# Performance work log

Measured on AMD Instinct MI355X. Metric: run time of the kernel, lower is better.

## Reference

```python
import jax, jax.numpy as jnp
import numpy as np

N_NODES = 50000
N_EDGES = 800000
N_HIDDEN = 64
N_LAYER = 3
IN_DIM = 4


def setup_inputs() -> dict:
    key = jax.random.key(0)
    ks = jax.random.split(key, 10)
    x = jax.random.normal(ks[0], (N_NODES, IN_DIM), dtype=jnp.float32)
    edge_index = jax.random.randint(ks[1], (2, N_EDGES), 0, N_NODES, dtype=jnp.int64)
    # Glorot-style params matching pyg GCNConv (lin has no bias; conv adds bias after aggregation)
    def glorot(k, fan_in, fan_out):
        s = jnp.sqrt(6.0 / (fan_in + fan_out))
        return jax.random.uniform(k, (fan_in, fan_out), jnp.float32, -s, s)
    W_in = glorot(ks[2], IN_DIM, N_HIDDEN)
    b_in = jnp.zeros((N_HIDDEN,), jnp.float32)
    W_h = jnp.stack([glorot(jax.random.fold_in(ks[3], i), N_HIDDEN, N_HIDDEN) for i in range(N_LAYER)])
    b_h = jnp.zeros((N_LAYER, N_HIDDEN), jnp.float32)
    W_out = glorot(ks[4], N_HIDDEN, 1)
    b_out = jnp.zeros((1,), jnp.float32)
    return {"x": x, "edge_index": edge_index, "W_in": W_in, "b_in": b_in,
            "W_h": W_h, "b_h": b_h, "W_out": W_out, "b_out": b_out}


def _gcn_norm(edge_index, n_nodes):
    # add self-loops, compute symmetric norm D^{-1/2} (A+I) D^{-1/2}
    loop = jnp.arange(n_nodes, dtype=edge_index.dtype)
    src = jnp.concatenate([edge_index[0], loop])
    dst = jnp.concatenate([edge_index[1], loop])
    deg = jax.ops.segment_sum(jnp.ones_like(dst, dtype=jnp.float32), dst, num_segments=n_nodes)
    dinv = jax.lax.rsqrt(deg)  # deg >= 1 due to self-loops
    norm = dinv[src] * dinv[dst]
    return src, dst, norm


def _gcn_conv(x, W, b, src, dst, norm, n_nodes):
    h = x @ W                                   # [N, out]
    msg = h[src] * norm[:, None]                # gather + scale, [E+N, out]
    out = jax.ops.segment_sum(msg, dst, num_segments=n_nodes)  # scatter-add
    return out + b


def reference(x, edge_index, W_in, b_in, W_h, b_h, W_out, b_out):
    n = x.shape[0]
    src, dst, norm = _gcn_norm(edge_index, n)
    h = jax.nn.relu(_gcn_conv(x, W_in, b_in, src, dst, norm, n))
    for i in range(W_h.shape[0]):
        h = jax.nn.relu(_gcn_conv(h, W_h[i], b_h[i], src, dst, norm, n))
    return _gcn_conv(h, W_out, b_out, src, dst, norm, n)
```

## Files before the change

kernel.cpp:

```cpp
#include <hip/hip_runtime.h>
#include <hip/hip_bf16.h>


#define TPB 256
#define EPT 8
#define CHUNK (TPB * EPT)
typedef __hip_bfloat16 bf16;
#define B2F __bfloat162float

__global__ void k_zero_b(int* __restrict__ bktcnt, int* __restrict__ ticket) {
    bktcnt[threadIdx.x] = 0;
    if (threadIdx.x == 0) *ticket = 0;
}

__global__ __launch_bounds__(TPB) void k_bktcnt(
    const int* __restrict__ dst, int* __restrict__ bktcnt, int* __restrict__ ticket,
    int* __restrict__ bktbase, int* __restrict__ bcur, int E, int n) {
    __shared__ int h[256];
    __shared__ int lastFlag;
    int tid = threadIdx.x;
    h[tid] = 0;
    __syncthreads();
    int e0 = blockIdx.x * CHUNK;
#pragma unroll
    for (int u = 0; u < EPT; ++u) {
        int e = e0 + u * TPB + tid;
        if (e < E) {
            int d = dst[e];
            if ((unsigned)d < (unsigned)n) atomicAdd(&h[d >> 8], 1);
        }
    }
    __syncthreads();
    if (h[tid]) atomicAdd(&bktcnt[tid], h[tid]);
    __threadfence();
    __syncthreads();
    if (tid == 0) lastFlag = (atomicAdd(ticket, 1) == (int)gridDim.x - 1);
    __syncthreads();
    if (!lastFlag) return;
    int v = atomicAdd(&bktcnt[tid], 0);
    h[tid] = v;
    __syncthreads();
    for (int off = 1; off < 256; off <<= 1) {
        int u2 = (tid >= off) ? h[tid - off] : 0;
        __syncthreads();
        h[tid] += u2;
        __syncthreads();
    }
    int excl = h[tid] - v;
    bktbase[tid] = excl;
    bcur[tid] = excl;
    if (tid == 255) bktbase[256] = h[tid];
}

__global__ __launch_bounds__(TPB) void k_bin(
    const int* __restrict__ src, const int* __restrict__ dst,
    int* __restrict__ bcur, unsigned* __restrict__ staging, int E, int n) {
    __shared__ int hcnt[256];
    __shared__ int hbase[256];
    int tid = threadIdx.x;
    int e0 = blockIdx.x * CHUNK;
    hcnt[tid] = 0;
    __syncthreads();

    int eb[EPT];
    unsigned rec[EPT];
#pragma unroll
    for (int u = 0; u < EPT; ++u) {
        int e = e0 + u * TPB + tid;
        eb[u] = -1;
        if (e < E) {
            int d = dst[e], s = src[e];
            if ((unsigned)d < (unsigned)n && (unsigned)s < (unsigned)n) {
                eb[u] = d >> 8;
                rec[u] = (unsigned)s | ((unsigned)(d & 255) << 16);
                atomicAdd(&hcnt[eb[u]], 1);
            }
        }
    }
    __syncthreads();
    int c = hcnt[tid];
    hbase[tid] = (c > 0) ? atomicAdd(&bcur[tid], c) : 0;
    hcnt[tid] = 0;
    __syncthreads();
#pragma unroll
    for (int u = 0; u < EPT; ++u) {
        if (eb[u] >= 0) {
            int r = atomicAdd(&hcnt[eb[u]], 1);
            int pos = hbase[eb[u]] + r;
            if ((unsigned)pos < (unsigned)E) staging[pos] = rec[u];
        }
    }
}

__global__ __launch_bounds__(TPB) void k_unbin2(
    const unsigned* __restrict__ staging, const int* __restrict__ bktbase,
    const float* __restrict__ x, float4* __restrict__ xt,
    int* __restrict__ row_start, float* __restrict__ dinv,
    unsigned short* __restrict__ bucket, int E, int n) {
    __shared__ int cnt[256];
    __shared__ int scn[256];
    __shared__ int cur[256];
    int b = blockIdx.x, tid = threadIdx.x;
    int lo = bktbase[b], hi = bktbase[b + 1];
    lo = max(0, min(lo, E)); hi = max(lo, min(hi, E));

    cnt[tid] = 0;
    __syncthreads();
    for (int i = lo + tid; i < hi; i += TPB)
        atomicAdd(&cnt[(staging[i] >> 16) & 255], 1);
    __syncthreads();

    int v = cnt[tid];
    scn[tid] = v;
    __syncthreads();
    for (int off = 1; off < 256; off <<= 1) {
        int u = (tid >= off) ? scn[tid - off] : 0;
        __syncthreads();
        scn[tid] += u;
        __syncthreads();
    }
    int excl = scn[tid] - v;
    int base = min(lo + excl, E);
    cur[tid] = base;
    int d = (b << 8) + tid;
    if (d < n) {
        row_start[d] = base;
        float di = rsqrtf((float)v + 1.0f);
        dinv[d] = di;
        float4 xv = ((const float4*)x)[d];
        xv.x *= di; xv.y *= di; xv.z *= di; xv.w *= di;
        xt[d] = xv;
        if (d == n - 1) row_start[n] = min(base + v, E);
    }
    __syncthreads();

    for (int i = lo + tid; i < hi; i += TPB) {
        unsigned r = staging[i];
        int t = (r >> 16) & 255;
        int pos = atomicAdd(&cur[t], 1);
        if ((unsigned)pos < (unsigned)E) bucket[pos] = (unsigned short)(r & 0xffffu);
    }
}

__device__ __forceinline__ void acc_oct(float* a, uint4 w) {
    a[0] += __uint_as_float(w.x << 16);
    a[1] += __uint_as_float(w.x & 0xffff0000u);
    a[2] += __uint_as_float(w.y << 16);
    a[3] += __uint_as_float(w.y & 0xffff0000u);
    a[4] += __uint_as_float(w.z << 16);
    a[5] += __uint_as_float(w.z & 0xffff0000u);
    a[6] += __uint_as_float(w.w << 16);
    a[7] += __uint_as_float(w.w & 0xffff0000u);
}

__device__ __forceinline__ void agg_oct(const bf16* __restrict__ g,
                                        const unsigned short* __restrict__ bucket,
                                        int k0, int k1, int d, float* __restrict__ a,
                                        int lane, unsigned nm1, unsigned Em1) {
    int grp = lane >> 3, i = lane & 7;
#pragma unroll
    for (int m = 0; m < 8; ++m) a[m] = 0.f;
    if (grp == 0) {
        uint4 w = *(const uint4*)(g + (size_t)d * 64 + 8 * i);
        acc_oct(a, w);
    }
    for (int base = k0; base < k1; base += 64) {
        int cnt = min(64, k1 - base);
        int rec = bucket[min((unsigned)(base + lane), Em1)];
        int k = 0;
        for (; k + 16 <= cnt; k += 16) {
            unsigned s0 = min((unsigned)__shfl(rec, k + grp), nm1);
            unsigned s1 = min((unsigned)__shfl(rec, k + 8 + grp), nm1);
            uint4 w0 = *(const uint4*)(g + (size_t)s0 * 64 + 8 * i);
            uint4 w1 = *(const uint4*)(g + (size_t)s1 * 64 + 8 * i);
            acc_oct(a, w0);
            acc_oct(a, w1);
        }
        for (; k < cnt; k += 8) {
            int e = k + grp;
            unsigned s = min((unsigned)__shfl(rec, min(e, 63)), nm1);
            uint4 w = *(const uint4*)(g + (size_t)s * 64 + 8 * i);
            if (e < cnt) acc_oct(a, w);
        }
    }
}

__global__ __launch_bounds__(TPB, 4) void k_gconv1(
    const float4* __restrict__ xt, const float* __restrict__ dinv,
    const int* __restrict__ row_start, const unsigned short* __restrict__ bucket,
    const float* __restrict__ W_in, const float* __restrict__ b_in,
    const float* __restrict__ Wh0, bf16* __restrict__ gOut, int n, int E) {
    __shared__ float sAct[4][64];
    int tid = threadIdx.x;
    int r = tid >> 6, j = tid & 63;
    unsigned nm1 = (unsigned)(n - 1);

    float wreg[64];
#pragma unroll
    for (int k = 0; k < 64; ++k) wreg[k] = Wh0[k * 64 + j];
    float win0 = W_in[0 * 64 + j], win1 = W_in[1 * 64 + j];
    float win2 = W_in[2 * 64 + j], win3 = W_in[3 * 64 + j];
    float bj = b_in[j];

    int nw = gridDim.x * 4;
    for (int d = blockIdx.x * 4 + r; d < n; d += nw) {
        float dd = dinv[d];
        int k0 = row_start[d], k1 = row_start[d + 1];
        k1 = min(k1, E); k0 = max(min(k0, k1), 0);

        float4 v = make_float4(0.f, 0.f, 0.f, 0.f);
        if (j == 0) v = xt[d];
        for (int k = k0 + j; k < k1; k += 64) {
            unsigned s = min((unsigned)bucket[k], nm1);
            float4 t = xt[s];
            v.x += t.x; v.y += t.y; v.z += t.z; v.w += t.w;
        }
#pragma unroll
        for (int off = 1; off < 64; off <<= 1) {
            v.x += __shfl_xor(v.x, off);
            v.y += __shfl_xor(v.y, off);
            v.z += __shfl_xor(v.z, off);
            v.w += __shfl_xor(v.w, off);
        }
        float dot = fmaf(v.x, win0, fmaf(v.y, win1, fmaf(v.z, win2, v.w * win3)));
        float act = fmaxf(fmaf(dd, dot, bj), 0.f);
        sAct[r][j] = act;

        float acc0 = 0.f, acc1 = 0.f, acc2 = 0.f, acc3 = 0.f;
        const float4* ap = (const float4*)&sAct[r][0];
#pragma unroll
        for (int k4 = 0; k4 < 16; ++k4) {
            float4 av = ap[k4];
            acc0 = fmaf(av.x, wreg[4 * k4 + 0], acc0);
            acc1 = fmaf(av.y, wreg[4 * k4 + 1], acc1);
            acc2 = fmaf(av.z, wreg[4 * k4 + 2], acc2);
            acc3 = fmaf(av.w, wreg[4 * k4 + 3], acc3);
        }
        float acc = (acc0 + acc1) + (acc2 + acc3);
        gOut[(size_t)d * 64 + j] = __float2bfloat16(acc * dd);
    }
}

__global__ __launch_bounds__(TPB, 4) void k_gconv(
    const bf16* __restrict__ gIn, const float* __restrict__ dinv,
    const int* __restrict__ row_start, const unsigned short* __restrict__ bucket,
    const float* __restrict__ bias, const float* __restrict__ W,
    bf16* __restrict__ gOut, int n, int E) {
    __shared__ float sVp[4][8][68];
    int tid = threadIdx.x;
    int r = tid >> 6, j = tid & 63;
    int grp = j >> 3, i = j & 7;
    unsigned nm1 = (unsigned)(n - 1), Em1 = (unsigned)(E - 1);

    float wreg[64];
#pragma unroll
    for (int k = 0; k < 64; ++k) wreg[k] = W[k * 64 + j];
    float bj = bias[j];

    int nw = gridDim.x * 4;
    for (int d = blockIdx.x * 4 + r; d < n; d += nw) {
        float dd = dinv[d];
        int k0 = row_start[d], k1 = row_start[d + 1];
        k1 = min(k1, E); k0 = max(min(k0, k1), 0);

        float a[8];
        agg_oct(gIn, bucket, k0, k1, d, a, j, nm1, Em1);

        float4* prow = (float4*)&sVp[r][grp][8 * i];
        prow[0] = make_float4(a[0], a[1], a[2], a[3]);
        prow[1] = make_float4(a[4], a[5], a[6], a[7]);
        float full = 0.f;
#pragma unroll
        for (int g = 0; g < 8; ++g) full += sVp[r][g][j];

        float act = fmaxf(fmaf(dd, full, bj), 0.f);
        sVp[r][0][j] = act;

        float acc0 = 0.f, acc1 = 0.f, acc2 = 0.f, acc3 = 0.f;
#pragma unroll
        for (int k4 = 0; k4 < 16; ++k4) {
            float4 av = *(const float4*)&sVp[r][0][4 * k4];
            acc0 = fmaf(av.x, wreg[4 * k4 + 0], acc0);
            acc1 = fmaf(av.y, wreg[4 * k4 + 1], acc1);
            acc2 = fmaf(av.z, wreg[4 * k4 + 2], acc2);
            acc3 = fmaf(av.w, wreg[4 * k4 + 3], acc3);
        }
        float acc = (acc0 + acc1) + (acc2 + acc3);
        gOut[(size_t)d * 64 + j] = __float2bfloat16(acc * dd);
    }
}

__global__ __launch_bounds__(TPB) void k_gconv_z(
    const bf16* __restrict__ gIn, const float* __restrict__ dinv,
    const int* __restrict__ row_start, const unsigned short* __restrict__ bucket,
    const float* __restrict__ bias, const float* __restrict__ Wout,
    float* __restrict__ zg, int n, int E) {
    __shared__ float sVp[4][8][68];
    int tid = threadIdx.x;
    int r = tid >> 6, j = tid & 63;
    int grp = j >> 3, i = j & 7;
    int d = blockIdx.x * 4 + r;
    if (d >= n) return;
    float dd = dinv[d];
    int k0 = row_start[d], k1 = row_start[d + 1];
    k1 = min(k1, E); k0 = max(min(k0, k1), 0);

    float a[8];
    agg_oct(gIn, bucket, k0, k1, d, a, j, (unsigned)(n - 1), (unsigned)(E - 1));

    float4* prow = (float4*)&sVp[r][grp][8 * i];
    prow[0] = make_float4(a[0], a[1], a[2], a[3]);
    prow[1] = make_float4(a[4], a[5], a[6], a[7]);
    float full = 0.f;
#pragma unroll
    for (int g = 0; g < 8; ++g) full += sVp[r][g][j];

    float p = fmaxf(fmaf(dd, full, bias[j]), 0.f) * Wout[j];
#pragma unroll
    for (int off = 32; off > 0; off >>= 1) p += __shfl_down(p, off);
    if (j == 0) zg[d] = p * dd;
}

__global__ __launch_bounds__(TPB) void k_out(
    const float* __restrict__ zg, const float* __restrict__ dinv,
    const int* __restrict__ row_start, const unsigned short* __restrict__ bucket,
    const float* __restrict__ b_out, float* __restrict__ out, int n, int E) {
    int t = blockIdx.x * blockDim.x + threadIdx.x;
    int d = t >> 6, lane = t & 63;
    if (d >= n) return;
    int k0 = row_start[d], k1 = row_start[d + 1];
    k1 = min(k1, E); k0 = max(min(k0, k1), 0);
    unsigned nm1 = (unsigned)(n - 1);
    float v = 0.f;
    for (int k = k0 + lane; k < k1; k += 64) {
        unsigned s = min((unsigned)bucket[k], nm1);
        v += zg[s];
    }
#pragma unroll
    for (int off = 32; off > 0; off >>= 1) v += __shfl_down(v, off);
    if (lane == 0) out[d] = fmaf(zg[d] + v, dinv[d], b_out[0]);
}

extern "C" void kernel_launch(void* const* d_in, const int* in_sizes, int n_in,
                              void* d_out, int out_size, void* d_ws, size_t ws_size,
                              hipStream_t stream) {
    const float* x     = (const float*)d_in[0];
    const int*   ei    = (const int*)d_in[1];
    const float* W_in  = (const float*)d_in[2];
    const float* b_in  = (const float*)d_in[3];
    const float* W_h   = (const float*)d_in[4];
    const float* b_h   = (const float*)d_in[5];
    const float* W_out = (const float*)d_in[6];
    const float* b_out = (const float*)d_in[7];
    float* out = (float*)d_out;

    int N = in_sizes[0] / 4;
    int E = in_sizes[1] / 2;
    const int* src = ei;
    const int* dst = ei + E;

    char* ws = (char*)d_ws;
    bf16* gA               = (bf16*)ws;           ws += (size_t)N * 64 * 2;
    bf16* gB               = (bf16*)ws;           ws += (size_t)N * 64 * 2;
    float4* xt             = (float4*)ws;         ws += (size_t)N * 16;
    unsigned short* bucket = (unsigned short*)ws; ws += (size_t)E * 2;
    unsigned* staging      = (unsigned*)ws;       ws += (size_t)E * 4;
    int*  row_start        = (int*)ws;            ws += (size_t)(N + 1) * 4;
    float* dinv            = (float*)ws;          ws += (size_t)N * 4;
    float* zg              = (float*)ws;          ws += (size_t)N * 4;
    int*  bktcnt           = (int*)ws;            ws += 256 * 4;
    int*  ticket           = (int*)ws;            ws += 4;
    int*  bktbase          = (int*)ws;            ws += 257 * 4;
    int*  bcur             = (int*)ws;

    int B     = (N + 255) >> 8;
    int gN4   = (N + 3) / 4;
    int gPers = 1024;
    int gBin  = (E + CHUNK - 1) / CHUNK;

    k_zero_b<<<1, 256, 0, stream>>>(bktcnt, ticket);
    k_bktcnt<<<gBin, TPB, 0, stream>>>(dst, bktcnt, ticket, bktbase, bcur, E, N);
    k_bin<<<gBin, TPB, 0, stream>>>(src, dst, bcur, staging, E, N);
    k_unbin2<<<B, TPB, 0, stream>>>(staging, bktbase, x, xt, row_start, dinv, bucket, E, N);

    k_gconv1<<<gPers, TPB, 0, stream>>>(xt, dinv, row_start, bucket, W_in, b_in, W_h, gB, N, E);
    k_gconv<<<gPers, TPB, 0, stream>>>(gB, dinv, row_start, bucket, b_h, W_h + 4096, gA, N, E);
    k_gconv<<<gPers, TPB, 0, stream>>>(gA, dinv, row_start, bucket, b_h + 64, W_h + 8192, gB, N, E);
    k_gconv_z<<<gN4, TPB, 0, stream>>>(gB, dinv, row_start, bucket, b_h + 128, W_out, zg, N, E);
    k_out<<<gN4, TPB, 0, stream>>>(zg, dinv, row_start, bucket, b_out, out, N, E);
}
```

Measured before the change: 260.0 us.

## Process two destination nodes per wavefront to overlap gather latency

Each wavefront in the hidden-layer and final aggregation kernels now handles a pair of destination nodes, interleaving their neighbor gathers so that four independent row loads are in flight per iteration instead of two. The aim is more memory-level parallelism on the latency-bound sparse gather. k_gconv_z also becomes a persistent grid-stride kernel with a fixed grid of 1024 blocks. The cost is higher register pressure from two accumulator sets, plus extra tail loops when the two nodes have different degrees.

Measured after the change: 413.1 us. 1.59x slower.

```diff
diff --git a/kernel.cpp b/kernel.cpp
--- a/kernel.cpp
+++ b/kernel.cpp
@@ -153,35 +153,77 @@
     a[7] += __uint_as_float(w.w & 0xffff0000u);
 }
 
-__device__ __forceinline__ void agg_oct(const bf16* __restrict__ g,
-                                        const unsigned short* __restrict__ bucket,
-                                        int k0, int k1, int d, float* __restrict__ a,
-                                        int lane, unsigned nm1, unsigned Em1) {
+__device__ __forceinline__ void agg_chunk(const bf16* __restrict__ g, int rec,
+                                          int kstart, int cnt, float* __restrict__ a,
+                                          int grp, int i, unsigned nm1) {
+    int k = kstart;
+    for (; k + 16 <= cnt; k += 16) {
+        unsigned s0 = min((unsigned)__shfl(rec, k + grp), nm1);
+        unsigned s1 = min((unsigned)__shfl(rec, k + 8 + grp), nm1);
+        uint4 w0 = *(const uint4*)(g + (size_t)s0 * 64 + 8 * i);
+        uint4 w1 = *(const uint4*)(g + (size_t)s1 * 64 + 8 * i);
+        acc_oct(a, w0);
+        acc_oct(a, w1);
+    }
+    for (; k < cnt; k += 8) {
+        int e = k + grp;
+        unsigned s = min((unsigned)__shfl(rec, min(e, 63)), nm1);
+        uint4 w = *(const uint4*)(g + (size_t)s * 64 + 8 * i);
+        if (e < cnt) acc_oct(a, w);
+    }
+}
+
+__device__ __forceinline__ void agg_oct2(const bf16* __restrict__ g,
+                                         const unsigned short* __restrict__ bucket,
+                                         int k0a, int k1a, int da,
+                                         int k0b, int k1b, int db, bool hasB,
+                                         float* __restrict__ aA, float* __restrict__ aB,
+                                         int lane, unsigned nm1, unsigned Em1) {
     int grp = lane >> 3, i = lane & 7;
 #pragma unroll
-    for (int m = 0; m < 8; ++m) a[m] = 0.f;
+    for (int m = 0; m < 8; ++m) { aA[m] = 0.f; aB[m] = 0.f; }
     if (grp == 0) {
-        uint4 w = *(const uint4*)(g + (size_t)d * 64 + 8 * i);
-        acc_oct(a, w);
-    }
-    for (int base = k0; base < k1; base += 64) {
-        int cnt = min(64, k1 - base);
-        int rec = bucket[min((unsigned)(base + lane), Em1)];
+        uint4 wa = *(const uint4*)(g + (size_t)da * 64 + 8 * i);
+        acc_oct(aA, wa);
+        if (hasB) {
+            uint4 wb = *(const uint4*)(g + (size_t)db * 64 + 8 * i);
+            acc_oct(aB, wb);
+        }
+    }
+    int bA = k0a, bB = k0b;
+    while (bA < k1a && bB < k1b) {
+        int cA = min(64, k1a - bA), cB = min(64, k1b - bB);
+        int recA = bucket[min((unsigned)(bA + lane), Em1)];
+        int recB = bucket[min((unsigned)(bB + lane), Em1)];
+        int cm = min(cA, cB);
         int k = 0;
-        for (; k + 16 <= cnt; k += 16) {
-            unsigned s0 = min((unsigned)__shfl(rec, k + grp), nm1);
-            unsigned s1 = min((unsigned)__shfl(rec, k + 8 + grp), nm1);
-            uint4 w0 = *(const uint4*)(g + (size_t)s0 * 64 + 8 * i);
-            uint4 w1 = *(const uint4*)(g + (size_t)s1 * 64 + 8 * i);
-            acc_oct(a, w0);
-            acc_oct(a, w1);
-        }
-        for (; k < cnt; k += 8) {
-            int e = k + grp;
-            unsigned s = min((unsigned)__shfl(rec, min(e, 63)), nm1);
-            uint4 w = *(const uint4*)(g + (size_t)s * 64 + 8 * i);
-            if (e < cnt) acc_oct(a, w);
-        }
+        for (; k + 16 <= cm; k += 16) {
+            unsigned s0a = min((unsigned)__shfl(recA, k + grp), nm1);
+            unsigned s1a = min((unsigned)__shfl(recA, k + 8 + grp), nm1);
+            unsigned s0b = min((unsigned)__shfl(recB, k + grp), nm1);
+            unsigned s1b = min((unsigned)__shfl(recB, k + 8 + grp), nm1);
+            uint4 w0a = *(const uint4*)(g + (size_t)s0a * 64 + 8 * i);
+            uint4 w1a = *(const uint4*)(g + (size_t)s1a * 64 + 8 * i);
+            uint4 w0b = *(const uint4*)(g + (size_t)s0b * 64 + 8 * i);
+            uint4 w1b = *(const uint4*)(g + (size_t)s1b * 64 + 8 * i);
+            acc_oct(aA, w0a);
+            acc_oct(aA, w1a);
+            acc_oct(aB, w0b);
+            acc_oct(aB, w1b);
+        }
+        agg_chunk(g, recA, k, cA, aA, grp, i, nm1);
+        agg_chunk(g, recB, k, cB, aB, grp, i, nm1);
+        bA += 64; bB += 64;
+    }
+    for (; bA < k1a; bA += 64) {
+        int cA = min(64, k1a - bA);
+        int recA = bucket[min((unsigned)(bA + lane), Em1)];
+        agg_chunk(g, recA, 0, cA, aA, grp, i, nm1);
+    }
+    for (; bB < k1b; bB += 64) {
+        int cB = min(64, k1b - bB);
+        int recB = bucket[min((unsigned)(bB + lane), Em1)];
+        agg_chunk(g, recB, 0, cB, aB, grp, i, nm1);
     }
 }
 
@@ -258,24 +300,33 @@
     float bj = bias[j];
 
     int nw = gridDim.x * 4;
-    for (int d = blockIdx.x * 4 + r; d < n; d += nw) {
-        float dd = dinv[d];
-        int k0 = row_start[d], k1 = row_start[d + 1];
-        k1 = min(k1, E); k0 = max(min(k0, k1), 0);
-
-        float a[8];
-        agg_oct(gIn, bucket, k0, k1, d, a, j, nm1, Em1);
+    int npair = (n + 1) >> 1;
+    for (int p = blockIdx.x * 4 + r; p < npair; p += nw) {
+        int dA = 2 * p, dB = dA + 1;
+        bool hasB = dB < n;
+        float ddA = dinv[dA];
+        int k0a = row_start[dA], k1a = row_start[dA + 1];
+        k1a = min(k1a, E); k0a = max(min(k0a, k1a), 0);
+        float ddB = 0.f;
+        int k0b = 0, k1b = 0;
+        if (hasB) {
+            ddB = dinv[dB];
+            k0b = row_start[dB]; k1b = row_start[dB + 1];
+            k1b = min(k1b, E); k0b = max(min(k0b, k1b), 0);
+        }
+
+        float aA[8], aB[8];
+        agg_oct2(gIn, bucket, k0a, k1a, dA, k0b, k1b, min(dB, n - 1), hasB,
+                 aA, aB, j, nm1, Em1);
 
         float4* prow = (float4*)&sVp[r][grp][8 * i];
-        prow[0] = make_float4(a[0], a[1], a[2], a[3]);
-        prow[1] = make_float4(a[4], a[5], a[6], a[7]);
+        prow[0] = make_float4(aA[0], aA[1], aA[2], aA[3]);
+        prow[1] = make_float4(aA[4], aA[5], aA[6], aA[7]);
         float full = 0.f;
 #pragma unroll
         for (int g = 0; g < 8; ++g) full += sVp[r][g][j];
-
-        float act = fmaxf(fmaf(dd, full, bj), 0.f);
+        float act = fmaxf(fmaf(ddA, full, bj), 0.f);
         sVp[r][0][j] = act;
-
         float acc0 = 0.f, acc1 = 0.f, acc2 = 0.f, acc3 = 0.f;
 #pragma unroll
         for (int k4 = 0; k4 < 16; ++k4) {
@@ -285,12 +336,31 @@
             acc2 = fmaf(av.z, wreg[4 * k4 + 2], acc2);
             acc3 = fmaf(av.w, wreg[4 * k4 + 3], acc3);
         }
-        float acc = (acc0 + acc1) + (acc2 + acc3);
-        gOut[(size_t)d * 64 + j] = __float2bfloat16(acc * dd);
-    }
-}
-
-__global__ __launch_bounds__(TPB) void k_gconv_z(
+        gOut[(size_t)dA * 64 + j] = __float2bfloat16(((acc0 + acc1) + (acc2 + acc3)) * ddA);
+
+        if (hasB) {
+            prow[0] = make_float4(aB[0], aB[1], aB[2], aB[3]);
+            prow[1] = make_float4(aB[4], aB[5], aB[6], aB[7]);
+            float fullB = 0.f;
+#pragma unroll
+            for (int g = 0; g < 8; ++g) fullB += sVp[r][g][j];
+            float actB = fmaxf(fmaf(ddB, fullB, bj), 0.f);
+            sVp[r][0][j] = actB;
+            float b0 = 0.f, b1 = 0.f, b2 = 0.f, b3 = 0.f;
+#pragma unroll
+            for (int k4 = 0; k4 < 16; ++k4) {
+                float4 av = *(const float4*)&sVp[r][0][4 * k4];
+                b0 = fmaf(av.x, wreg[4 * k4 + 0], b0);
+                b1 = fmaf(av.y, wreg[4 * k4 + 1], b1);
+                b2 = fmaf(av.z, wreg[4 * k4 + 2], b2);
+                b3 = fmaf(av.w, wreg[4 * k4 + 3], b3);
+            }
+            gOut[(size_t)dB * 64 + j] = __float2bfloat16(((b0 + b1) + (b2 + b3)) * ddB);
+        }
+    }
+}
+
+__global__ __launch_bounds__(TPB, 4) void k_gconv_z(
     const bf16* __restrict__ gIn, const float* __restrict__ dinv,
     const int* __restrict__ row_start, const unsigned short* __restrict__ bucket,
     const float* __restrict__ bias, const float* __restrict__ Wout,
@@ -299,26 +369,52 @@
     int tid = threadIdx.x;
     int r = tid >> 6, j = tid & 63;
     int grp = j >> 3, i = j & 7;
-    int d = blockIdx.x * 4 + r;
-    if (d >= n) return;
-    float dd = dinv[d];
-    int k0 = row_start[d], k1 = row_start[d + 1];
-    k1 = min(k1, E); k0 = max(min(k0, k1), 0);
-
-    float a[8];
-    agg_oct(gIn, bucket, k0, k1, d, a, j, (unsigned)(n - 1), (unsigned)(E - 1));
-
-    float4* prow = (float4*)&sVp[r][grp][8 * i];
-    prow[0] = make_float4(a[0], a[1], a[2], a[3]);
-    prow[1] = make_float4(a[4], a[5], a[6], a[7]);
-    float full = 0.f;
-#pragma unroll
-    for (int g = 0; g < 8; ++g) full += sVp[r][g][j];
-
-    float p = fmaxf(fmaf(dd, full, bias[j]), 0.f) * Wout[j];
-#pragma unroll
-    for (int off = 32; off > 0; off >>= 1) p += __shfl_down(p, off);
-    if (j == 0) zg[d] = p * dd;
+    unsigned nm1 = (unsigned)(n - 1), Em1 = (unsigned)(E - 1);
+    float bj = bias[j], wj = Wout[j];
+
+    int nw = gridDim.x * 4;
+    int npair = (n + 1) >> 1;
+    for (int p = blockIdx.x * 4 + r; p < npair; p += nw) {
+        int dA = 2 * p, dB = dA + 1;
+        bool hasB = dB < n;
+        float ddA = dinv[dA];
+        int k0a = row_start[dA], k1a = row_start[dA + 1];
+        k1a = min(k1a, E); k0a = max(min(k0a, k1a), 0);
+        float ddB = 0.f;
+        int k0b = 0, k1b = 0;
+        if (hasB) {
+            ddB = dinv[dB];
+            k0b = row_start[dB]; k1b = row_start[dB + 1];
+            k1b = min(k1b, E); k0b = max(min(k0b, k1b), 0);
+        }
+
+        float aA[8], aB[8];
+        agg_oct2(gIn, bucket, k0a, k1a, dA, k0b, k1b, min(dB, n - 1), hasB,
+                 aA, aB, j, nm1, Em1);
+
+        float4* prow = (float4*)&sVp[r][grp][8 * i];
+        prow[0] = make_float4(aA[0], aA[1], aA[2], aA[3]);
+        prow[1] = make_float4(aA[4], aA[5], aA[6], aA[7]);
+        float full = 0.f;
+#pragma unroll
+        for (int g = 0; g < 8; ++g) full += sVp[r][g][j];
+        float pA = fmaxf(fmaf(ddA, full, bj), 0.f) * wj;
+#pragma unroll
+        for (int off = 32; off > 0; off >>= 1) pA += __shfl_down(pA, off);
+        if (j == 0) zg[dA] = pA * ddA;
+
+        if (hasB) {
+            prow[0] = make_float4(aB[0], aB[1], aB[2], aB[3]);
+            prow[1] = make_float4(aB[4], aB[5], aB[6], aB[7]);
+            float fullB = 0.f;
+#pragma unroll
+            for (int g = 0; g < 8; ++g) fullB += sVp[r][g][j];
+            float pB = fmaxf(fmaf(ddB, fullB, bj), 0.f) * wj;
+#pragma unroll
+            for (int off = 32; off > 0; off >>= 1) pB += __shfl_down(pB, off);
+            if (j == 0) zg[dB] = pB * ddB;
+        }
+    }
 }
 
 __global__ __launch_bounds__(TPB) void k_out(
@@ -386,6 +482,6 @@
     k_gconv1<<<gPers, TPB, 0, stream>>>(xt, dinv, row_start, bucket, W_in, b_in, W_h, gB, N, E);
     k_gconv<<<gPers, TPB, 0, stream>>>(gB, dinv, row_start, bucket, b_h, W_h + 4096, gA, N, E);
     k_gconv<<<gPers, TPB, 0, stream>>>(gA, dinv, row_start, bucket, b_h + 64, W_h + 8192, gB, N, E);
-    k_gconv_z<<<gN4, TPB, 0, stream>>>(gB, dinv, row_start, bucket, b_h + 128, W_out, zg, N, E);
+    k_gconv_z<<<gPers, TPB, 0, stream>>>(gB, dinv, row_start, bucket, b_h + 128, W_out, zg, N, E);
     k_out<<<gN4, TPB, 0, stream>>>(zg, dinv, row_start, bucket, b_out, out, N, E);
 }
```

## Pack weights to bf16 registers, shuffle-reduce aggregates, raise occupancy

Applied to the files above, without the earlier changes.

Keeps the per-thread 64-wide weight column packed as bf16 pairs, halving the register footprint, and raises launch bounds and persistent grid sizes so more waves fit per CU. The shared-memory cross-group reduction of aggregated features is replaced by wave shuffles. The final layer kernel becomes persistent. Rounding the hidden weights to bf16 adds precision loss in the matmuls.

After: 419.3 us. 61.3% more time.

```diff
diff --git a/kernel.cpp b/kernel.cpp
--- a/kernel.cpp
+++ b/kernel.cpp
@@ -153,6 +153,14 @@
     a[7] += __uint_as_float(w.w & 0xffff0000u);
 }
 
+__device__ __forceinline__ unsigned pk_bf2(float lo, float hi) {
+    unsigned a = __float_as_uint(lo);
+    unsigned b = __float_as_uint(hi);
+    a = (a + 0x7fffu + ((a >> 16) & 1u)) >> 16;
+    b = (b + 0x7fffu + ((b >> 16) & 1u)) & 0xffff0000u;
+    return b | (a & 0xffffu);
+}
+
 __device__ __forceinline__ void agg_oct(const bf16* __restrict__ g,
                                         const unsigned short* __restrict__ bucket,
                                         int k0, int k1, int d, float* __restrict__ a,
@@ -185,7 +193,7 @@
     }
 }
 
-__global__ __launch_bounds__(TPB, 4) void k_gconv1(
+__global__ __launch_bounds__(TPB, 6) void k_gconv1(
     const float4* __restrict__ xt, const float* __restrict__ dinv,
     const int* __restrict__ row_start, const unsigned short* __restrict__ bucket,
     const float* __restrict__ W_in, const float* __restrict__ b_in,
@@ -195,9 +203,10 @@
     int r = tid >> 6, j = tid & 63;
     unsigned nm1 = (unsigned)(n - 1);
 
-    float wreg[64];
-#pragma unroll
-    for (int k = 0; k < 64; ++k) wreg[k] = Wh0[k * 64 + j];
+    unsigned wbf[32];
+#pragma unroll
+    for (int k2 = 0; k2 < 32; ++k2)
+        wbf[k2] = pk_bf2(Wh0[(2 * k2) * 64 + j], Wh0[(2 * k2 + 1) * 64 + j]);
     float win0 = W_in[0 * 64 + j], win1 = W_in[1 * 64 + j];
     float win2 = W_in[2 * 64 + j], win3 = W_in[3 * 64 + j];
     float bj = b_in[j];
@@ -226,36 +235,38 @@
         float act = fmaxf(fmaf(dd, dot, bj), 0.f);
         sAct[r][j] = act;
 
-        float acc0 = 0.f, acc1 = 0.f, acc2 = 0.f, acc3 = 0.f;
+        float acc0 = 0.f, acc1 = 0.f;
         const float4* ap = (const float4*)&sAct[r][0];
 #pragma unroll
         for (int k4 = 0; k4 < 16; ++k4) {
             float4 av = ap[k4];
-            acc0 = fmaf(av.x, wreg[4 * k4 + 0], acc0);
-            acc1 = fmaf(av.y, wreg[4 * k4 + 1], acc1);
-            acc2 = fmaf(av.z, wreg[4 * k4 + 2], acc2);
-            acc3 = fmaf(av.w, wreg[4 * k4 + 3], acc3);
-        }
-        float acc = (acc0 + acc1) + (acc2 + acc3);
-        gOut[(size_t)d * 64 + j] = __float2bfloat16(acc * dd);
-    }
-}
-
-__global__ __launch_bounds__(TPB, 4) void k_gconv(
+            unsigned wA = wbf[2 * k4], wB = wbf[2 * k4 + 1];
+            acc0 = fmaf(av.x, __uint_as_float(wA << 16), acc0);
+            acc1 = fmaf(av.y, __uint_as_float(wA & 0xffff0000u), acc1);
+            acc0 = fmaf(av.z, __uint_as_float(wB << 16), acc0);
+            acc1 = fmaf(av.w, __uint_as_float(wB & 0xffff0000u), acc1);
+        }
+        gOut[(size_t)d * 64 + j] = __float2bfloat16((acc0 + acc1) * dd);
+    }
+}
+
+__global__ __launch_bounds__(TPB, 6) void k_gconv(
     const bf16* __restrict__ gIn, const float* __restrict__ dinv,
     const int* __restrict__ row_start, const unsigned short* __restrict__ bucket,
     const float* __restrict__ bias, const float* __restrict__ W,
     bf16* __restrict__ gOut, int n, int E) {
-    __shared__ float sVp[4][8][68];
+    __shared__ float sAct[4][64];
     int tid = threadIdx.x;
     int r = tid >> 6, j = tid & 63;
     int grp = j >> 3, i = j & 7;
     unsigned nm1 = (unsigned)(n - 1), Em1 = (unsigned)(E - 1);
 
-    float wreg[64];
-#pragma unroll
-    for (int k = 0; k < 64; ++k) wreg[k] = W[k * 64 + j];
-    float bj = bias[j];
+    unsigned wbf[32];
+#pragma unroll
+    for (int k2 = 0; k2 < 32; ++k2)
+        wbf[k2] = pk_bf2(W[(2 * k2) * 64 + j], W[(2 * k2 + 1) * 64 + j]);
+    const float4* b4 = (const float4*)bias;
+    float4 bA = b4[2 * i], bB = b4[2 * i + 1];
 
     int nw = gridDim.x * 4;
     for (int d = blockIdx.x * 4 + r; d < n; d += nw) {
@@ -266,59 +277,81 @@
         float a[8];
         agg_oct(gIn, bucket, k0, k1, d, a, j, nm1, Em1);
 
-        float4* prow = (float4*)&sVp[r][grp][8 * i];
-        prow[0] = make_float4(a[0], a[1], a[2], a[3]);
-        prow[1] = make_float4(a[4], a[5], a[6], a[7]);
-        float full = 0.f;
-#pragma unroll
-        for (int g = 0; g < 8; ++g) full += sVp[r][g][j];
-
-        float act = fmaxf(fmaf(dd, full, bj), 0.f);
-        sVp[r][0][j] = act;
-
-        float acc0 = 0.f, acc1 = 0.f, acc2 = 0.f, acc3 = 0.f;
+#pragma unroll
+        for (int m = 0; m < 8; ++m) {
+            a[m] += __shfl_xor(a[m], 8);
+            a[m] += __shfl_xor(a[m], 16);
+            a[m] += __shfl_xor(a[m], 32);
+        }
+        if (grp == 0) {
+            float4 r0, r1;
+            r0.x = fmaxf(fmaf(dd, a[0], bA.x), 0.f);
+            r0.y = fmaxf(fmaf(dd, a[1], bA.y), 0.f);
+            r0.z = fmaxf(fmaf(dd, a[2], bA.z), 0.f);
+            r0.w = fmaxf(fmaf(dd, a[3], bA.w), 0.f);
+            r1.x = fmaxf(fmaf(dd, a[4], bB.x), 0.f);
+            r1.y = fmaxf(fmaf(dd, a[5], bB.y), 0.f);
+            r1.z = fmaxf(fmaf(dd, a[6], bB.z), 0.f);
+            r1.w = fmaxf(fmaf(dd, a[7], bB.w), 0.f);
+            float4* arow = (float4*)&sAct[r][8 * i];
+            arow[0] = r0; arow[1] = r1;
+        }
+        float acc0 = 0.f, acc1 = 0.f;
+        const float4* ap = (const float4*)&sAct[r][0];
 #pragma unroll
         for (int k4 = 0; k4 < 16; ++k4) {
-            float4 av = *(const float4*)&sVp[r][0][4 * k4];
-            acc0 = fmaf(av.x, wreg[4 * k4 + 0], acc0);
-            acc1 = fmaf(av.y, wreg[4 * k4 + 1], acc1);
-            acc2 = fmaf(av.z, wreg[4 * k4 + 2], acc2);
-            acc3 = fmaf(av.w, wreg[4 * k4 + 3], acc3);
-        }
-        float acc = (acc0 + acc1) + (acc2 + acc3);
-        gOut[(size_t)d * 64 + j] = __float2bfloat16(acc * dd);
-    }
-}
-
-__global__ __launch_bounds__(TPB) void k_gconv_z(
+            float4 av = ap[k4];
+            unsigned wA = wbf[2 * k4], wB = wbf[2 * k4 + 1];
+            acc0 = fmaf(av.x, __uint_as_float(wA << 16), acc0);
+            acc1 = fmaf(av.y, __uint_as_float(wA & 0xffff0000u), acc1);
+            acc0 = fmaf(av.z, __uint_as_float(wB << 16), acc0);
+            acc1 = fmaf(av.w, __uint_as_float(wB & 0xffff0000u), acc1);
+        }
+        gOut[(size_t)d * 64 + j] = __float2bfloat16((acc0 + acc1) * dd);
+    }
+}
+
+__global__ __launch_bounds__(TPB, 8) void k_gconv_z(
     const bf16* __restrict__ gIn, const float* __restrict__ dinv,
     const int* __restrict__ row_start, const unsigned short* __restrict__ bucket,
     const float* __restrict__ bias, const float* __restrict__ Wout,
     float* __restrict__ zg, int n, int E) {
-    __shared__ float sVp[4][8][68];
     int tid = threadIdx.x;
     int r = tid >> 6, j = tid & 63;
-    int grp = j >> 3, i = j & 7;
-    int d = blockIdx.x * 4 + r;
-    if (d >= n) return;
-    float dd = dinv[d];
-    int k0 = row_start[d], k1 = row_start[d + 1];
-    k1 = min(k1, E); k0 = max(min(k0, k1), 0);
-
-    float a[8];
-    agg_oct(gIn, bucket, k0, k1, d, a, j, (unsigned)(n - 1), (unsigned)(E - 1));
-
-    float4* prow = (float4*)&sVp[r][grp][8 * i];
-    prow[0] = make_float4(a[0], a[1], a[2], a[3]);
-    prow[1] = make_float4(a[4], a[5], a[6], a[7]);
-    float full = 0.f;
-#pragma unroll
-    for (int g = 0; g < 8; ++g) full += sVp[r][g][j];
-
-    float p = fmaxf(fmaf(dd, full, bias[j]), 0.f) * Wout[j];
-#pragma unroll
-    for (int off = 32; off > 0; off >>= 1) p += __shfl_down(p, off);
-    if (j == 0) zg[d] = p * dd;
+    int i = j & 7;
+    unsigned nm1 = (unsigned)(n - 1), Em1 = (unsigned)(E - 1);
+    const float4* b4 = (const float4*)bias;
+    const float4* w4 = (const float4*)Wout;
+    float4 bA = b4[2 * i], bB = b4[2 * i + 1];
+    float4 wA = w4[2 * i], wB = w4[2 * i + 1];
+
+    int nw = gridDim.x * 4;
+    for (int d = blockIdx.x * 4 + r; d < n; d += nw) {
+        float dd = dinv[d];
+        int k0 = row_start[d], k1 = row_start[d + 1];
+        k1 = min(k1, E); k0 = max(min(k0, k1), 0);
+
+        float a[8];
+        agg_oct(gIn, bucket, k0, k1, d, a, j, nm1, Em1);
+#pragma unroll
+        for (int m = 0; m < 8; ++m) {
+            a[m] += __shfl_xor(a[m], 8);
+            a[m] += __shfl_xor(a[m], 16);
+            a[m] += __shfl_xor(a[m], 32);
+        }
+        float p = fmaxf(fmaf(dd, a[0], bA.x), 0.f) * wA.x
+                + fmaxf(fmaf(dd, a[1], bA.y), 0.f) * wA.y
+                + fmaxf(fmaf(dd, a[2], bA.z), 0.f) * wA.z
+                + fmaxf(fmaf(dd, a[3], bA.w), 0.f) * wA.w
+                + fmaxf(fmaf(dd, a[4], bB.x), 0.f) * wB.x
+                + fmaxf(fmaf(dd, a[5], bB.y), 0.f) * wB.y
+                + fmaxf(fmaf(dd, a[6], bB.z), 0.f) * wB.z
+                + fmaxf(fmaf(dd, a[7], bB.w), 0.f) * wB.w;
+        p += __shfl_xor(p, 1);
+        p += __shfl_xor(p, 2);
+        p += __shfl_xor(p, 4);
+        if (j == 0) zg[d] = p * dd;
+    }
 }
 
 __global__ __launch_bounds__(TPB) void k_out(
@@ -375,7 +408,8 @@
 
     int B     = (N + 255) >> 8;
     int gN4   = (N + 3) / 4;
-    int gPers = 1024;
+    int gP6   = 1536;
+    int gP8   = 2048;
     int gBin  = (E + CHUNK - 1) / CHUNK;
 
     k_zero_b<<<1, 256, 0, stream>>>(bktcnt, ticket);
@@ -383,9 +417,9 @@
     k_bin<<<gBin, TPB, 0, stream>>>(src, dst, bcur, staging, E, N);
     k_unbin2<<<B, TPB, 0, stream>>>(staging, bktbase, x, xt, row_start, dinv, bucket, E, N);
 
-    k_gconv1<<<gPers, TPB, 0, stream>>>(xt, dinv, row_start, bucket, W_in, b_in, W_h, gB, N, E);
-    k_gconv<<<gPers, TPB, 0, stream>>>(gB, dinv, row_start, bucket, b_h, W_h + 4096, gA, N, E);
-    k_gconv<<<gPers, TPB, 0, stream>>>(gA, dinv, row_start, bucket, b_h + 64, W_h + 8192, gB, N, E);
-    k_gconv_z<<<gN4, TPB, 0, stream>>>(gB, dinv, row_start, bucket, b_h + 128, W_out, zg, N, E);
+    k_gconv1<<<gP6, TPB, 0, stream>>>(xt, dinv, row_start, bucket, W_in, b_in, W_h, gB, N, E);
+    k_gconv<<<gP6, TPB, 0, stream>>>(gB, dinv, row_start, bucket, b_h, W_h + 4096, gA, N, E);
+    k_gconv<<<gP6, TPB, 0, stream>>>(gA, dinv, row_start, bucket, b_h + 64, W_h + 8192, gB, N, E);
+    k_gconv_z<<<gP8, TPB, 0, stream>>>(gB, dinv, row_start, bucket, b_h + 128, W_out, zg, N, E);
     k_out<<<gN4, TPB, 0, stream>>>(zg, dinv, row_start, bucket, b_out, out, N, E);
 }
```

## Pack hidden weights as bf16 pairs to cut registers and raise occupancy

Applied to the files above, without the earlier changes.

Adds a small kernel that packs each hidden-layer weight matrix into bf16 pairs, so each thread holds 32 packed registers instead of 64 float weights. The gconv kernels unpack the pairs with shifts and masks in the matmul loop, and their launch bounds and persistent grid size go from 4 to 6 blocks per CU. The aim is more resident waves to hide gather latency. In exchange it adds unpack ALU ops, one extra kernel launch, and a loss of weight precision from rounding to bf16.

Measured after the change: 378.8 us. 1.46x slower.

```diff
diff --git a/kernel.cpp b/kernel.cpp
--- a/kernel.cpp
+++ b/kernel.cpp
@@ -11,6 +11,24 @@
 __global__ void k_zero_b(int* __restrict__ bktcnt, int* __restrict__ ticket) {
     bktcnt[threadIdx.x] = 0;
     if (threadIdx.x == 0) *ticket = 0;
+}
+
+__device__ __forceinline__ unsigned pk_bf2(float lo, float hi) {
+    unsigned a = __float_as_uint(lo);
+    unsigned b = __float_as_uint(hi);
+    a = (a + 0x7fffu + ((a >> 16) & 1u)) >> 16;
+    b = (b + 0x7fffu + ((b >> 16) & 1u)) & 0xffff0000u;
+    return b | (a & 0xffffu);
+}
+
+__global__ __launch_bounds__(TPB) void k_pack(const float* __restrict__ Wh,
+                                              unsigned* __restrict__ wpk) {
+    int t = blockIdx.x * blockDim.x + threadIdx.x;
+    if (t >= 3 * 2048) return;
+    int l = t >> 11, idx = t & 2047;
+    int k2 = idx >> 6, j = idx & 63;
+    const float* W = Wh + l * 4096;
+    wpk[t] = pk_bf2(W[(2 * k2) * 64 + j], W[(2 * k2 + 1) * 64 + j]);
 }
 
 __global__ __launch_bounds__(TPB) void k_bktcnt(
@@ -185,19 +203,19 @@
     }
 }
 
-__global__ __launch_bounds__(TPB, 4) void k_gconv1(
+__global__ __launch_bounds__(TPB, 6) void k_gconv1(
     const float4* __restrict__ xt, const float* __restrict__ dinv,
     const int* __restrict__ row_start, const unsigned short* __restrict__ bucket,
     const float* __restrict__ W_in, const float* __restrict__ b_in,
-    const float* __restrict__ Wh0, bf16* __restrict__ gOut, int n, int E) {
+    const unsigned* __restrict__ wpk0, bf16* __restrict__ gOut, int n, int E) {
     __shared__ float sAct[4][64];
     int tid = threadIdx.x;
     int r = tid >> 6, j = tid & 63;
     unsigned nm1 = (unsigned)(n - 1);
 
-    float wreg[64];
-#pragma unroll
-    for (int k = 0; k < 64; ++k) wreg[k] = Wh0[k * 64 + j];
+    unsigned wbf[32];
+#pragma unroll
+    for (int k2 = 0; k2 < 32; ++k2) wbf[k2] = wpk0[k2 * 64 + j];
     float win0 = W_in[0 * 64 + j], win1 = W_in[1 * 64 + j];
     float win2 = W_in[2 * 64 + j], win3 = W_in[3 * 64 + j];
     float bj = b_in[j];
@@ -226,25 +244,25 @@
         float act = fmaxf(fmaf(dd, dot, bj), 0.f);
         sAct[r][j] = act;
 
-        float acc0 = 0.f, acc1 = 0.f, acc2 = 0.f, acc3 = 0.f;
+        float acc0 = 0.f, acc1 = 0.f;
         const float4* ap = (const float4*)&sAct[r][0];
 #pragma unroll
         for (int k4 = 0; k4 < 16; ++k4) {
             float4 av = ap[k4];
-            acc0 = fmaf(av.x, wreg[4 * k4 + 0], acc0);
-            acc1 = fmaf(av.y, wreg[4 * k4 + 1], acc1);
-            acc2 = fmaf(av.z, wreg[4 * k4 + 2], acc2);
-            acc3 = fmaf(av.w, wreg[4 * k4 + 3], acc3);
-        }
-        float acc = (acc0 + acc1) + (acc2 + acc3);
-        gOut[(size_t)d * 64 + j] = __float2bfloat16(acc * dd);
-    }
-}
-
-__global__ __launch_bounds__(TPB, 4) void k_gconv(
+            unsigned wA = wbf[2 * k4], wB = wbf[2 * k4 + 1];
+            acc0 = fmaf(av.x, __uint_as_float(wA << 16), acc0);
+            acc1 = fmaf(av.y, __uint_as_float(wA & 0xffff0000u), acc1);
+            acc0 = fmaf(av.z, __uint_as_float(wB << 16), acc0);
+            acc1 = fmaf(av.w, __uint_as_float(wB & 0xffff0000u), acc1);
+        }
+        gOut[(size_t)d * 64 + j] = __float2bfloat16((acc0 + acc1) * dd);
+    }
+}
+
+__global__ __launch_bounds__(TPB, 6) void k_gconv(
     const bf16* __restrict__ gIn, const float* __restrict__ dinv,
     const int* __restrict__ row_start, const unsigned short* __restrict__ bucket,
-    const float* __restrict__ bias, const float* __restrict__ W,
+    const float* __restrict__ bias, const unsigned* __restrict__ wpk,
     bf16* __restrict__ gOut, int n, int E) {
     __shared__ float sVp[4][8][68];
     int tid = threadIdx.x;
@@ -252,9 +270,9 @@
     int grp = j >> 3, i = j & 7;
     unsigned nm1 = (unsigned)(n - 1), Em1 = (unsigned)(E - 1);
 
-    float wreg[64];
-#pragma unroll
-    for (int k = 0; k < 64; ++k) wreg[k] = W[k * 64 + j];
+    unsigned wbf[32];
+#pragma unroll
+    for (int k2 = 0; k2 < 32; ++k2) wbf[k2] = wpk[k2 * 64 + j];
     float bj = bias[j];
 
     int nw = gridDim.x * 4;
@@ -276,17 +294,17 @@
         float act = fmaxf(fmaf(dd, full, bj), 0.f);
         sVp[r][0][j] = act;
 
-        float acc0 = 0.f, acc1 = 0.f, acc2 = 0.f, acc3 = 0.f;
+        float acc0 = 0.f, acc1 = 0.f;
 #pragma unroll
         for (int k4 = 0; k4 < 16; ++k4) {
             float4 av = *(const float4*)&sVp[r][0][4 * k4];
-            acc0 = fmaf(av.x, wreg[4 * k4 + 0], acc0);
-            acc1 = fmaf(av.y, wreg[4 * k4 + 1], acc1);
-            acc2 = fmaf(av.z, wreg[4 * k4 + 2], acc2);
-            acc3 = fmaf(av.w, wreg[4 * k4 + 3], acc3);
-        }
-        float acc = (acc0 + acc1) + (acc2 + acc3);
-        gOut[(size_t)d * 64 + j] = __float2bfloat16(acc * dd);
+            unsigned wA = wbf[2 * k4], wB = wbf[2 * k4 + 1];
+            acc0 = fmaf(av.x, __uint_as_float(wA << 16), acc0);
+            acc1 = fmaf(av.y, __uint_as_float(wA & 0xffff0000u), acc1);
+            acc0 = fmaf(av.z, __uint_as_float(wB << 16), acc0);
+            acc1 = fmaf(av.w, __uint_as_float(wB & 0xffff0000u), acc1);
+        }
+        gOut[(size_t)d * 64 + j] = __float2bfloat16((acc0 + acc1) * dd);
     }
 }
 
@@ -368,6 +386,7 @@
     int*  row_start        = (int*)ws;            ws += (size_t)(N + 1) * 4;
     float* dinv            = (float*)ws;          ws += (size_t)N * 4;
     float* zg              = (float*)ws;          ws += (size_t)N * 4;
+    unsigned* wpk          = (unsigned*)ws;       ws += 3 * 2048 * 4;
     int*  bktcnt           = (int*)ws;            ws += 256 * 4;
     int*  ticket           = (int*)ws;            ws += 4;
     int*  bktbase          = (int*)ws;            ws += 257 * 4;
@@ -375,17 +394,18 @@
 
     int B     = (N + 255) >> 8;
     int gN4   = (N + 3) / 4;
-    int gPers = 1024;
+    int gP6   = 1536;
     int gBin  = (E + CHUNK - 1) / CHUNK;
 
     k_zero_b<<<1, 256, 0, stream>>>(bktcnt, ticket);
+    k_pack<<<24, TPB, 0, stream>>>(W_h, wpk);
     k_bktcnt<<<gBin, TPB, 0, stream>>>(dst, bktcnt, ticket, bktbase, bcur, E, N);
     k_bin<<<gBin, TPB, 0, stream>>>(src, dst, bcur, staging, E, N);
     k_unbin2<<<B, TPB, 0, stream>>>(staging, bktbase, x, xt, row_start, dinv, bucket, E, N);
 
-    k_gconv1<<<gPers, TPB, 0, stream>>>(xt, dinv, row_start, bucket, W_in, b_in, W_h, gB, N, E);
-    k_gconv<<<gPers, TPB, 0, stream>>>(gB, dinv, row_start, bucket, b_h, W_h + 4096, gA, N, E);
-    k_gconv<<<gPers, TPB, 0, stream>>>(gA, dinv, row_start, bucket, b_h + 64, W_h + 8192, gB, N, E);
+    k_gconv1<<<gP6, TPB, 0, stream>>>(xt, dinv, row_start, bucket, W_in, b_in, wpk, gB, N, E);
+    k_gconv<<<gP6, TPB, 0, stream>>>(gB, dinv, row_start, bucket, b_h, wpk + 2048, gA, N, E);
+    k_gconv<<<gP6, TPB, 0, stream>>>(gA, dinv, row_start, bucket, b_h + 64, wpk + 4096, gB, N, E);
     k_gconv_z<<<gN4, TPB, 0, stream>>>(gB, dinv, row_start, bucket, b_h + 128, W_out, zg, N, E);
     k_out<<<gN4, TPB, 0, stream>>>(zg, dinv, row_start, bucket, b_out, out, N, E);
 }
```
